# Kernel optimization log

Measured on AMD Instinct MI355X. Metric: run time of the kernel, lower is better.

## Reference

```python
import jax, jax.numpy as jnp
import numpy as np

B, S, D, H = 4, 2048, 1024, 16
HD = D // H
EPS = 1e-5


def gelu_tanh(x):
    c = jnp.sqrt(jnp.asarray(2.0 / jnp.pi, x.dtype))
    return x * 0.5 * (1.0 + jnp.tanh(c * (x + 0.044715 * x ** 3)))


def layer_norm(x, scale, shift):
    mean = jnp.mean(x, axis=-1, keepdims=True)
    var = jnp.var(x, axis=-1, keepdims=True)  # unbiased=False
    return scale * ((x - mean) / jnp.sqrt(var + EPS)) + shift


def setup_inputs() -> dict:
    key = jax.random.key(0)
    ks = jax.random.split(key, 8)
    s = 0.02
    return {
        "x": jax.random.normal(ks[0], (B, S, D), jnp.float32),
        "Wqkv": jax.random.normal(ks[1], (D, 3 * D), jnp.float32) * s,
        "Wout": jax.random.normal(ks[2], (D, D), jnp.float32) * s,
        "bout": jnp.zeros((D,), jnp.float32),
        "W1": jax.random.normal(ks[3], (D, 4 * D), jnp.float32) * s,
        "b1": jnp.zeros((4 * D,), jnp.float32),
        "W2": jax.random.normal(ks[4], (4 * D, D), jnp.float32) * s,
        "b2": jnp.zeros((D,), jnp.float32),
        "g1": jnp.ones((D,), jnp.float32),
        "s1": jnp.zeros((D,), jnp.float32),
        "g2": jnp.ones((D,), jnp.float32),
        "s2": jnp.zeros((D,), jnp.float32),
    }


def reference(x, Wqkv, Wout, bout, W1, b1, W2, b2, g1, s1, g2, s2):
    # --- attention branch ---
    h = layer_norm(x, g1, s1)
    qkv = h @ Wqkv  # [B,S,3D]
    qkv = qkv.reshape(B, S, 3, H, HD).transpose(2, 0, 3, 1, 4)  # [3,B,H,S,hd]
    q, k, v = qkv[0], qkv[1], qkv[2]
    scores = jnp.einsum("bhqd,bhkd->bhqk", q, k)
    causal = jnp.triu(jnp.ones((S, S), bool), k=1)
    scores = jnp.where(causal, -jnp.inf, scores)
    attn = jax.nn.softmax(scores / jnp.sqrt(jnp.asarray(HD, x.dtype)), axis=-1)
    ctx = jnp.einsum("bhqk,bhkd->bhqd", attn, v)
    ctx = ctx.transpose(0, 2, 1, 3).reshape(B, S, D)
    x = x + (ctx @ Wout + bout)
    # --- MLP branch ---
    h = layer_norm(x, g2, s2)
    h = gelu_tanh(h @ W1 + b1) @ W2 + b2
    return x + h
```

## Files before the change

### kernel.cpp

```cpp
#include <hip/hip_runtime.h>
#include <stdint.h>

typedef unsigned short u16;
typedef unsigned long long u64;
typedef __attribute__((ext_vector_type(8))) short bf16x8;
typedef __attribute__((ext_vector_type(4))) float f32x4;

#define DEV __device__ __forceinline__

DEV u16 f2bf(float f) {
  union { float f; unsigned u; } v; v.f = f;
  unsigned r = (v.u + 0x7fffu + ((v.u >> 16) & 1u)) >> 16;
  return (u16)r;
}

#define GLDS(g, l) __builtin_amdgcn_global_load_lds( \
    (const __attribute__((address_space(1))) void*)(g), \
    (__attribute__((address_space(3))) void*)(l), 16, 0, 0)

#define BAR() __builtin_amdgcn_s_barrier()
#define LGKM0() asm volatile("s_waitcnt lgkmcnt(0)" ::: "memory")
#define VMW(n) asm volatile("s_waitcnt vmcnt(" #n ")" ::: "memory")
#define SCHED0() __builtin_amdgcn_sched_barrier(0)

__global__ __launch_bounds__(256) void k_transpose_all(
    const float* __restrict__ Wqkv, const float* __restrict__ Wout,
    const float* __restrict__ W1, const float* __restrict__ W2,
    u16* __restrict__ WqkvT, u16* __restrict__ WoutT,
    u16* __restrict__ W1T, u16* __restrict__ W2T) {
  int id = blockIdx.x;
  const float* in; u16* out; int K, N, nx, base;
  if (id < 3072)      { in = Wqkv; out = WqkvT; K = 1024; N = 3072; nx = 96;  base = 0; }
  else if (id < 4096) { in = Wout; out = WoutT; K = 1024; N = 1024; nx = 32;  base = 3072; }
  else if (id < 8192) { in = W1;   out = W1T;   K = 1024; N = 4096; nx = 128; base = 4096; }
  else                { in = W2;   out = W2T;   K = 4096; N = 1024; nx = 32;  base = 8192; }
  int seg = id - base, bx = seg % nx, by = seg / nx;
  __shared__ float tile[32][33];
  int tx = threadIdx.x & 31, ty = threadIdx.x >> 5;
#pragma unroll
  for (int r = 0; r < 32; r += 8)
    tile[ty + r][tx] = in[(size_t)(by * 32 + ty + r) * N + bx * 32 + tx];
  __syncthreads();
#pragma unroll
  for (int r = 0; r < 32; r += 8)
    out[(size_t)(bx * 32 + ty + r) * K + by * 32 + tx] = f2bf(tile[tx][ty + r]);
}

__global__ __launch_bounds__(256) void k_layernorm(
    const float* __restrict__ x, const float* __restrict__ gamma,
    const float* __restrict__ beta, u16* __restrict__ out) {
  int row = blockIdx.x, t = threadIdx.x;
  const float4 v = ((const float4*)(x + (size_t)row * 1024))[t];
  float sum = v.x + v.y + v.z + v.w;
  float sq = v.x * v.x + v.y * v.y + v.z * v.z + v.w * v.w;
#pragma unroll
  for (int o = 32; o >= 1; o >>= 1) {
    sum += __shfl_down(sum, o);
    sq += __shfl_down(sq, o);
  }
  __shared__ float red[8];
  if ((t & 63) == 0) { red[(t >> 6) * 2] = sum; red[(t >> 6) * 2 + 1] = sq; }
  __syncthreads();
  sum = red[0] + red[2] + red[4] + red[6];
  sq = red[1] + red[3] + red[5] + red[7];
  float mean = sum * (1.0f / 1024.0f);
  float var = sq * (1.0f / 1024.0f) - mean * mean;
  float rstd = rsqrtf(var + 1e-5f);
  float4 g = ((const float4*)gamma)[t];
  float4 b = ((const float4*)beta)[t];
  ushort4 o4;
  o4.x = f2bf(g.x * (v.x - mean) * rstd + b.x);
  o4.y = f2bf(g.y * (v.y - mean) * rstd + b.y);
  o4.z = f2bf(g.z * (v.z - mean) * rstd + b.z);
  o4.w = f2bf(g.w * (v.w - mean) * rstd + b.w);
  ((ushort4*)(out + (size_t)row * 1024))[t] = o4;
}

struct EpiQKV {
  u16 *Q, *K2, *VT;
  DEV void operator()(int r, int c0, const f32x4& v) const {
    int three = c0 >> 10, h = (c0 >> 6) & 15, hd = c0 & 63;
    int b = r >> 11, s = r & 2047;
    int bh = b * 16 + h;
    ushort4 o;
    o.x = f2bf(v[0]); o.y = f2bf(v[1]); o.z = f2bf(v[2]); o.w = f2bf(v[3]);
    if (three == 0)
      *(ushort4*)&Q[((size_t)bh * 2048 + s) * 64 + hd] = o;
    else if (three == 1)
      *(ushort4*)&K2[((size_t)bh * 2048 + s) * 64 + hd] = o;
    else {
      VT[((size_t)bh * 64 + hd + 0) * 2048 + s] = o.x;
      VT[((size_t)bh * 64 + hd + 1) * 2048 + s] = o.y;
      VT[((size_t)bh * 64 + hd + 2) * 2048 + s] = o.z;
      VT[((size_t)bh * 64 + hd + 3) * 2048 + s] = o.w;
    }
  }
};

struct EpiBiasResid {
  const float* bias; const float* resid; float* out; int N;
  DEV void operator()(int r, int c0, const f32x4& v) const {
    size_t idx = (size_t)r * N + c0;
    float4 bb = *(const float4*)&bias[c0];
    float4 rr = *(const float4*)&resid[idx];
    float4 o;
    o.x = v[0] + bb.x + rr.x; o.y = v[1] + bb.y + rr.y;
    o.z = v[2] + bb.z + rr.z; o.w = v[3] + bb.w + rr.w;
    *(float4*)&out[idx] = o;
  }
};

struct EpiBiasGelu {
  const float* bias; u16* out; int N;
  DEV float gelu(float xx) const {
    float u = 0.7978845608f * (xx + 0.044715f * xx * xx * xx);
    float e = __expf(2.0f * u);
    float th = 1.0f - 2.0f / (e + 1.0f);
    return 0.5f * xx * (1.0f + th);
  }
  DEV void operator()(int r, int c0, const f32x4& v) const {
    float4 bb = *(const float4*)&bias[c0];
    ushort4 o;
    o.x = f2bf(gelu(v[0] + bb.x)); o.y = f2bf(gelu(v[1] + bb.y));
    o.z = f2bf(gelu(v[2] + bb.z)); o.w = f2bf(gelu(v[3] + bb.w));
    *(ushort4*)&out[(size_t)r * N + c0] = o;
  }
};

#define STG8(tk, d) do { \
    GLDS(gA + (tk) * 64,                        &As[d][0][t * 8]); \
    GLDS(gA + (tk) * 64 + (size_t)64 * K,       &As[d][0][t * 8 + 2048]); \
    GLDS(gA + (tk) * 64 + 32,                   &As[d][1][t * 8]); \
    GLDS(gA + (tk) * 64 + 32 + (size_t)64 * K,  &As[d][1][t * 8 + 2048]); \
    GLDS(gB + (tk) * 64,                        &Bs[d][0][t * 8]); \
    GLDS(gB + (tk) * 64 + (size_t)64 * K,       &Bs[d][0][t * 8 + 2048]); \
    GLDS(gB + (tk) * 64 + 32,                   &Bs[d][1][t * 8]); \
    GLDS(gB + (tk) * 64 + 32 + (size_t)64 * K,  &Bs[d][1][t * 8 + 2048]); \
  } while (0)

template <typename Epi>
__global__ __launch_bounds__(256) void k_gemm_tn(
    const u16* __restrict__ A, const u16* __restrict__ Bt, int K, Epi epi) {
  __shared__ u16 As[2][2][128 * 32];
  __shared__ u16 Bs[2][2][128 * 32];
  const int t = threadIdx.x;
  const int bm = blockIdx.x, bn = blockIdx.y;
  const int lane = t & 63, w = t >> 6;
  const int wm = w >> 1, wn = w & 1;
  const int quad = lane >> 4, l16 = lane & 15;
  f32x4 acc[4][4] = {};
  const u16* gA = A + (size_t)(bm * 128 + (t >> 2)) * K + (t & 3) * 8;
  const u16* gB = Bt + (size_t)(bn * 128 + (t >> 2)) * K + (t & 3) * 8;
  const int NT = K >> 6;

  STG8(0, 0);
  STG8(1, 1);
  VMW(8);
  BAR();

  for (int T = 0; T < NT; ++T) {
    const int d = T & 1;
#pragma unroll
    for (int kk = 0; kk < 2; ++kk) {
      bf16x8 af[4], bfr[4];
#pragma unroll
      for (int mt = 0; mt < 4; ++mt)
        af[mt] = *(const bf16x8*)&As[d][kk][(wm * 64 + mt * 16 + l16) * 32 + quad * 8];
#pragma unroll
      for (int nt = 0; nt < 4; ++nt)
        bfr[nt] = *(const bf16x8*)&Bs[d][kk][(wn * 64 + nt * 16 + l16) * 32 + quad * 8];
#pragma unroll
      for (int mt = 0; mt < 4; ++mt)
#pragma unroll
        for (int nt = 0; nt < 4; ++nt)
          acc[mt][nt] = __builtin_amdgcn_mfma_f32_16x16x32_bf16(
              bfr[nt], af[mt], acc[mt][nt], 0, 0, 0);
    }
    SCHED0();
    BAR();
    SCHED0();
    if (T + 2 < NT) {
      STG8(T + 2, d);
      VMW(8);
    } else {
      VMW(0);
    }
    BAR();
  }

  const int r0 = bm * 128 + wm * 64 + l16;
  const int c0 = bn * 128 + wn * 64 + quad * 4;
#pragma unroll
  for (int mt = 0; mt < 4; ++mt)
#pragma unroll
    for (int nt = 0; nt < 4; ++nt)
      epi(r0 + mt * 16, c0 + nt * 16, acc[mt][nt]);
}

#define STG8W(tk, d) do { \
    GLDS(gA + (tk) * 64,                         &As[d][0][t * 8]); \
    GLDS(gA + (tk) * 64 + (size_t)128 * K,       &As[d][0][t * 8 + 4096]); \
    GLDS(gA + (tk) * 64 + 32,                    &As[d][1][t * 8]); \
    GLDS(gA + (tk) * 64 + 32 + (size_t)128 * K,  &As[d][1][t * 8 + 4096]); \
    GLDS(gB + (tk) * 64,                         &Bs[d][0][t * 8]); \
    GLDS(gB + (tk) * 64 + (size_t)128 * K,       &Bs[d][0][t * 8 + 4096]); \
    GLDS(gB + (tk) * 64 + 32,                    &Bs[d][1][t * 8]); \
    GLDS(gB + (tk) * 64 + 32 + (size_t)128 * K,  &Bs[d][1][t * 8 + 4096]); \
  } while (0)

template <typename Epi>
__global__ __launch_bounds__(512, 2) void k_gemm_wide(
    const u16* __restrict__ A, const u16* __restrict__ Bt, int K, Epi epi) {
  __shared__ u16 As[2][2][256 * 32];
  __shared__ u16 Bs[2][2][256 * 32];
  const int t = threadIdx.x;
  const int bm = blockIdx.x, bn = blockIdx.y;
  const int lane = t & 63, w = t >> 6;
  const int wm = w >> 2, wn = w & 3;
  const int quad = lane >> 4, l16 = lane & 15;
  f32x4 acc[8][4] = {};
  const u16* gA = A + (size_t)(bm * 256 + (t >> 2)) * K + (t & 3) * 8;
  const u16* gB = Bt + (size_t)(bn * 256 + (t >> 2)) * K + (t & 3) * 8;
  const int NT = K >> 6;

  STG8W(0, 0);
  STG8W(1, 1);
  VMW(8);
  BAR();

  for (int T = 0; T < NT; ++T) {
    const int d = T & 1;
#pragma unroll
    for (int kk = 0; kk < 2; ++kk) {
      bf16x8 af[8], bfr[4];
#pragma unroll
      for (int mt = 0; mt < 8; ++mt)
        af[mt] = *(const bf16x8*)&As[d][kk][(wm * 128 + mt * 16 + l16) * 32 + quad * 8];
#pragma unroll
      for (int nt = 0; nt < 4; ++nt)
        bfr[nt] = *(const bf16x8*)&Bs[d][kk][(wn * 64 + nt * 16 + l16) * 32 + quad * 8];
#pragma unroll
      for (int mt = 0; mt < 8; ++mt)
#pragma unroll
        for (int nt = 0; nt < 4; ++nt)
          acc[mt][nt] = __builtin_amdgcn_mfma_f32_16x16x32_bf16(
              bfr[nt], af[mt], acc[mt][nt], 0, 0, 0);
    }
    SCHED0();
    BAR();
    SCHED0();
    if (T + 2 < NT) {
      STG8W(T + 2, d);
      VMW(8);
    } else {
      VMW(0);
    }
    BAR();
  }

  const int r0 = bm * 256 + wm * 128 + l16;
  const int c0 = bn * 256 + wn * 64 + quad * 4;
#pragma unroll
  for (int mt = 0; mt < 8; ++mt)
#pragma unroll
    for (int nt = 0; nt < 4; ++nt)
      epi(r0 + mt * 16, c0 + nt * 16, acc[mt][nt]);
}

#define PW 72

#define ATT_LOAD(kr, vr, k0_) do { \
  _Pragma("unroll") for (int j = 0; j < 4; ++j) { \
    int ch = t + 256 * j, r = ch >> 4, cc = (ch & 15) * 4; \
    kr[j] = *(const u64*)(Kbase + (size_t)((k0_) + r) * 64 + cc); \
    vr[j] = *(const u64*)(Vbase + (size_t)r * 2048 + (k0_) + cc); \
  } } while (0)

#define ATT_WRITE(kr, vr) do { \
  _Pragma("unroll") for (int j = 0; j < 4; ++j) { \
    int ch = t + 256 * j, r = ch >> 4, cc = (ch & 15) * 4; \
    *(u64*)&Ks[r * PW + cc] = kr[j]; \
    *(u64*)&Vs[r * PW + cc] = vr[j]; \
  } } while (0)

__global__ __launch_bounds__(256) void k_attn(
    const u16* __restrict__ Qg, const u16* __restrict__ Kg,
    const u16* __restrict__ VTg, u16* __restrict__ ctx) {
  const int bh = blockIdx.x;
  const int qt = 31 - blockIdx.y;
  const int b = bh >> 4, h = bh & 15;
  const int t = threadIdx.x, lane = t & 63, w = t >> 6;
  const int quad = lane >> 4, l16 = lane & 15;
  const int q0 = qt * 64;
  __shared__ u16 Qs[64 * PW], Ks[64 * PW], Vs[64 * PW];
  __shared__ u16 Ps[4][16 * PW];
  __shared__ float l_lds[4][16];
  const u16* Qbase = Qg + (size_t)bh * (2048 * 64);
  const u16* Kbase = Kg + (size_t)bh * (2048 * 64);
  const u16* Vbase = VTg + (size_t)bh * (64 * 2048);
#pragma unroll
  for (int j = 0; j < 4; ++j) {
    int ch = t + 256 * j, r = ch >> 4, cc = (ch & 15) * 4;
    *(u64*)&Qs[r * PW + cc] = *(const u64*)(Qbase + (size_t)(q0 + r) * 64 + cc);
  }
  __syncthreads();
  bf16x8 qf0 = *(const bf16x8*)&Qs[(w * 16 + l16) * PW + quad * 8];
  bf16x8 qf1 = *(const bf16x8*)&Qs[(w * 16 + l16) * PW + 32 + quad * 8];
  const int qrow = q0 + w * 16 + l16;
  const float c1 = 0.18033688011f;
  float lsum = 0.f;
  f32x4 acco[4] = {};

  auto tile = [&](int kt) {
    const int k0 = kt * 64;
    f32x4 sacc[4] = {};
#pragma unroll
    for (int kk = 0; kk < 2; ++kk) {
      bf16x8 qf = kk ? qf1 : qf0;
#pragma unroll
      for (int nt = 0; nt < 4; ++nt) {
        bf16x8 kf = *(const bf16x8*)&Ks[(nt * 16 + l16) * PW + kk * 32 + quad * 8];
        sacc[nt] = __builtin_amdgcn_mfma_f32_16x16x32_bf16(kf, qf, sacc[nt], 0, 0, 0);
      }
    }
    const bool diag = (kt == qt);
    float ls = 0.f;
#pragma unroll
    for (int nt = 0; nt < 4; ++nt) {
      ushort4 o;
#pragma unroll
      for (int reg = 0; reg < 4; ++reg) {
        float p = __builtin_amdgcn_exp2f(sacc[nt][reg] * c1);
        if (diag && (k0 + nt * 16 + quad * 4 + reg > qrow)) p = 0.f;
        ls += p;
        (&o.x)[reg] = f2bf(p);
      }
      *(ushort4*)&Ps[w][l16 * PW + nt * 16 + quad * 4] = o;
    }
    ls += __shfl_xor(ls, 16);
    ls += __shfl_xor(ls, 32);
    lsum += ls;
#pragma unroll
    for (int kk = 0; kk < 2; ++kk) {
      bf16x8 pf = *(const bf16x8*)&Ps[w][l16 * PW + kk * 32 + quad * 8];
#pragma unroll
      for (int nt = 0; nt < 4; ++nt) {
        bf16x8 vf = *(const bf16x8*)&Vs[(nt * 16 + l16) * PW + kk * 32 + quad * 8];
        acco[nt] = __builtin_amdgcn_mfma_f32_16x16x32_bf16(pf, vf, acco[nt], 0, 0, 0);
      }
    }
  };

  u64 kra[4], vra[4], krb[4], vrb[4];
  ATT_LOAD(kra, vra, 0);
  int kt = 0;
  while (true) {
    VMW(0);
    BAR();
    ATT_WRITE(kra, vra);
    if (kt + 1 <= qt) ATT_LOAD(krb, vrb, (kt + 1) * 64);
    LGKM0();
    BAR();
    tile(kt);
    if (++kt > qt) break;
    VMW(0);
    BAR();
    ATT_WRITE(krb, vrb);
    if (kt + 1 <= qt) ATT_LOAD(kra, vra, (kt + 1) * 64);
    LGKM0();
    BAR();
    tile(kt);
    if (++kt > qt) break;
  }

  if (quad == 0) l_lds[w][l16] = lsum;
  float4 lv = *(const float4*)&l_lds[w][quad * 4];
  float inv[4];
  inv[0] = 1.0f / lv.x; inv[1] = 1.0f / lv.y;
  inv[2] = 1.0f / lv.z; inv[3] = 1.0f / lv.w;
#pragma unroll
  for (int nt = 0; nt < 4; ++nt)
#pragma unroll
    for (int reg = 0; reg < 4; ++reg) {
      float o = acco[nt][reg] * inv[reg];
      int q = q0 + w * 16 + quad * 4 + reg;
      ctx[((size_t)(b * 2048 + q)) * 1024 + h * 64 + nt * 16 + l16] = f2bf(o);
    }
}

extern "C" void kernel_launch(void* const* d_in, const int* in_sizes, int n_in,
                              void* d_out, int out_size, void* d_ws, size_t ws_size,
                              hipStream_t stream) {
  (void)in_sizes; (void)n_in; (void)out_size; (void)ws_size;
  const float* x    = (const float*)d_in[0];
  const float* Wqkv = (const float*)d_in[1];
  const float* Wout = (const float*)d_in[2];
  const float* bout = (const float*)d_in[3];
  const float* W1   = (const float*)d_in[4];
  const float* b1   = (const float*)d_in[5];
  const float* W2   = (const float*)d_in[6];
  const float* b2   = (const float*)d_in[7];
  const float* g1   = (const float*)d_in[8];
  const float* s1   = (const float*)d_in[9];
  const float* g2   = (const float*)d_in[10];
  const float* s2   = (const float*)d_in[11];

  char* ws = (char*)d_ws;
  u16*   WqkvT = (u16*)(ws + 0);
  u16*   WoutT = (u16*)(ws + 6291456);
  u16*   W1T   = (u16*)(ws + 8388608);
  u16*   W2T   = (u16*)(ws + 16777216);
  float* x1    = (float*)(ws + 25165824);
  u16*   h12   = (u16*)(ws + 58720256);
  u16*   Qb    = (u16*)(ws + 75497472);
  u16*   Kb    = (u16*)(ws + 92274688);
  u16*   VTb   = (u16*)(ws + 109051904);
  u16*   ctx   = (u16*)(ws + 125829120);
  u16*   a1    = (u16*)(ws + 75497472);

  k_transpose_all<<<12288, 256, 0, stream>>>(Wqkv, Wout, W1, W2,
                                             WqkvT, WoutT, W1T, W2T);

  k_layernorm<<<8192, 256, 0, stream>>>(x, g1, s1, h12);
  k_gemm_wide<<<dim3(32, 12), 512, 0, stream>>>(h12, WqkvT, 1024,
                                                EpiQKV{Qb, Kb, VTb});
  k_attn<<<dim3(64, 32), 256, 0, stream>>>(Qb, Kb, VTb, ctx);
  k_gemm_tn<<<dim3(64, 8), 256, 0, stream>>>(ctx, WoutT, 1024,
                                             EpiBiasResid{bout, x, x1, 1024});
  k_layernorm<<<8192, 256, 0, stream>>>(x1, g2, s2, h12);
  k_gemm_wide<<<dim3(32, 16), 512, 0, stream>>>(h12, W1T, 1024,
                                                EpiBiasGelu{b1, a1, 4096});
  k_gemm_tn<<<dim3(64, 8), 256, 0, stream>>>(a1, W2T, 4096,
                                             EpiBiasResid{b2, x1, (float*)d_out, 1024});
}
```

Baseline: 530.1 us.

## Stage two key/value tiles per barrier in attention and use narrower GEMM for QKV

Result: faster. 516.6 us (-2.5%).

```diff
diff --git a/kernel.cpp b/kernel.cpp
--- a/kernel.cpp
+++ b/kernel.cpp
@@ -269,15 +269,17 @@
 
 #define PW 72
 
-#define ATT_LOAD(kr, vr, k0_) do { \
-  _Pragma("unroll") for (int j = 0; j < 4; ++j) { \
+#define ATT_LOAD128(kr, vr, k0_) do { \
+  _Pragma("unroll") for (int j = 0; j < 8; ++j) { \
     int ch = t + 256 * j, r = ch >> 4, cc = (ch & 15) * 4; \
-    kr[j] = *(const u64*)(Kbase + (size_t)((k0_) + r) * 64 + cc); \
-    vr[j] = *(const u64*)(Vbase + (size_t)r * 2048 + (k0_) + cc); \
+    int krow = (k0_) + r; krow = krow < 2047 ? krow : 2047; \
+    int vbase = (k0_) + (r >> 6) * 64; vbase = vbase < 1984 ? vbase : 1984; \
+    kr[j] = *(const u64*)(Kbase + (size_t)krow * 64 + cc); \
+    vr[j] = *(const u64*)(Vbase + (size_t)(r & 63) * 2048 + vbase + cc); \
   } } while (0)
 
-#define ATT_WRITE(kr, vr) do { \
-  _Pragma("unroll") for (int j = 0; j < 4; ++j) { \
+#define ATT_WRITE128(kr, vr) do { \
+  _Pragma("unroll") for (int j = 0; j < 8; ++j) { \
     int ch = t + 256 * j, r = ch >> 4, cc = (ch & 15) * 4; \
     *(u64*)&Ks[r * PW + cc] = kr[j]; \
     *(u64*)&Vs[r * PW + cc] = vr[j]; \
@@ -292,7 +294,7 @@
   const int t = threadIdx.x, lane = t & 63, w = t >> 6;
   const int quad = lane >> 4, l16 = lane & 15;
   const int q0 = qt * 64;
-  __shared__ u16 Qs[64 * PW], Ks[64 * PW], Vs[64 * PW];
+  __shared__ u16 Ks[128 * PW], Vs[128 * PW];
   __shared__ u16 Ps[4][16 * PW];
   __shared__ float l_lds[4][16];
   const u16* Qbase = Qg + (size_t)bh * (2048 * 64);
@@ -301,17 +303,18 @@
 #pragma unroll
   for (int j = 0; j < 4; ++j) {
     int ch = t + 256 * j, r = ch >> 4, cc = (ch & 15) * 4;
-    *(u64*)&Qs[r * PW + cc] = *(const u64*)(Qbase + (size_t)(q0 + r) * 64 + cc);
+    *(u64*)&Ks[r * PW + cc] = *(const u64*)(Qbase + (size_t)(q0 + r) * 64 + cc);
   }
   __syncthreads();
-  bf16x8 qf0 = *(const bf16x8*)&Qs[(w * 16 + l16) * PW + quad * 8];
-  bf16x8 qf1 = *(const bf16x8*)&Qs[(w * 16 + l16) * PW + 32 + quad * 8];
+  bf16x8 qf0 = *(const bf16x8*)&Ks[(w * 16 + l16) * PW + quad * 8];
+  bf16x8 qf1 = *(const bf16x8*)&Ks[(w * 16 + l16) * PW + 32 + quad * 8];
+  LGKM0();
   const int qrow = q0 + w * 16 + l16;
   const float c1 = 0.18033688011f;
   float lsum = 0.f;
   f32x4 acco[4] = {};
 
-  auto tile = [&](int kt) {
+  auto tile = [&](int kt, int off) {
     const int k0 = kt * 64;
     f32x4 sacc[4] = {};
 #pragma unroll
@@ -319,7 +322,7 @@
       bf16x8 qf = kk ? qf1 : qf0;
 #pragma unroll
       for (int nt = 0; nt < 4; ++nt) {
-        bf16x8 kf = *(const bf16x8*)&Ks[(nt * 16 + l16) * PW + kk * 32 + quad * 8];
+        bf16x8 kf = *(const bf16x8*)&Ks[(off + nt * 16 + l16) * PW + kk * 32 + quad * 8];
         sacc[nt] = __builtin_amdgcn_mfma_f32_16x16x32_bf16(kf, qf, sacc[nt], 0, 0, 0);
       }
     }
@@ -345,32 +348,23 @@
       bf16x8 pf = *(const bf16x8*)&Ps[w][l16 * PW + kk * 32 + quad * 8];
 #pragma unroll
       for (int nt = 0; nt < 4; ++nt) {
-        bf16x8 vf = *(const bf16x8*)&Vs[(nt * 16 + l16) * PW + kk * 32 + quad * 8];
+        bf16x8 vf = *(const bf16x8*)&Vs[(off + nt * 16 + l16) * PW + kk * 32 + quad * 8];
         acco[nt] = __builtin_amdgcn_mfma_f32_16x16x32_bf16(pf, vf, acco[nt], 0, 0, 0);
       }
     }
   };
 
-  u64 kra[4], vra[4], krb[4], vrb[4];
-  ATT_LOAD(kra, vra, 0);
-  int kt = 0;
-  while (true) {
+  u64 kr[8], vr[8];
+  ATT_LOAD128(kr, vr, 0);
+  for (int p0 = 0; p0 <= qt; p0 += 2) {
     VMW(0);
     BAR();
-    ATT_WRITE(kra, vra);
-    if (kt + 1 <= qt) ATT_LOAD(krb, vrb, (kt + 1) * 64);
+    ATT_WRITE128(kr, vr);
+    if (p0 + 2 <= qt) ATT_LOAD128(kr, vr, (p0 + 2) * 64);
     LGKM0();
     BAR();
-    tile(kt);
-    if (++kt > qt) break;
-    VMW(0);
-    BAR();
-    ATT_WRITE(krb, vrb);
-    if (kt + 1 <= qt) ATT_LOAD(kra, vra, (kt + 1) * 64);
-    LGKM0();
-    BAR();
-    tile(kt);
-    if (++kt > qt) break;
+    tile(p0, 0);
+    if (p0 + 1 <= qt) tile(p0 + 1, 64);
   }
 
   if (quad == 0) l_lds[w][l16] = lsum;
@@ -422,8 +416,8 @@
                                              WqkvT, WoutT, W1T, W2T);
 
   k_layernorm<<<8192, 256, 0, stream>>>(x, g1, s1, h12);
-  k_gemm_wide<<<dim3(32, 12), 512, 0, stream>>>(h12, WqkvT, 1024,
-                                                EpiQKV{Qb, Kb, VTb});
+  k_gemm_tn<<<dim3(64, 24), 256, 0, stream>>>(h12, WqkvT, 1024,
+                                              EpiQKV{Qb, Kb, VTb});
   k_attn<<<dim3(64, 32), 256, 0, stream>>>(Qb, Kb, VTb, ctx);
   k_gemm_tn<<<dim3(64, 8), 256, 0, stream>>>(ctx, WoutT, 1024,
                                              EpiBiasResid{bout, x, x1, 1024});
```
